# Optimization experiments

Hardware: AMD Instinct MI355X
Metric: run time of the kernel (lower is better)

The kernel has to match this reference:

```python
import jax, jax.numpy as jnp
import numpy as np

L, N, D, E, KD = 4, 40000, 128, 320000, 16
DECAY, N_ITER, EPS = 0.5, 3, 1e-5


def setup_inputs() -> dict:
    key = jax.random.key(0)
    ks = jax.random.split(key, 16)
    s = 0.05
    return {
        "x": jax.random.normal(ks[0], (L, N, D), jnp.float32),
        "edge_rows": jax.random.randint(ks[1], (E,), 0, N, jnp.int32),
        "edge_cols": jax.random.randint(ks[2], (E,), 0, N, jnp.int32),
        "edge_vals": jax.random.uniform(ks[3], (E,), jnp.float32) * 0.1,
        "sage_W": jax.random.normal(ks[4], (D, D), jnp.float32) * s,
        "sage_b": jnp.zeros((D,), jnp.float32),
        "sage_agg_W": jax.random.normal(ks[5], (D, D), jnp.float32) * s,
        "key_W": jax.random.normal(ks[6], (D, KD), jnp.float32) * s,
        "query_W": jax.random.normal(ks[7], (D, KD), jnp.float32) * s,
        "value_W": jax.random.normal(ks[8], (D, D), jnp.float32) * s,
        "attn_ln_g": jnp.ones((D,), jnp.float32),
        "attn_ln_b": jnp.zeros((D,), jnp.float32),
        "lin_W": jax.random.normal(ks[9], (D, D), jnp.float32) * s,
        "lin_b": jnp.zeros((D,), jnp.float32),
        "ln_g": jnp.ones((D,), jnp.float32),
        "ln_b": jnp.zeros((D,), jnp.float32),
    }


def _layernorm(x, g, b):
    mu = jnp.mean(x, axis=-1, keepdims=True)
    var = jnp.mean((x - mu) ** 2, axis=-1, keepdims=True)
    return (x - mu) * jax.lax.rsqrt(var + EPS) * g + b


def _spmm(rows, cols, vals, x2d):
    # sparse [N,N] @ dense [N,F]: out[r] = sum_e vals[e] * x2d[cols[e]] for rows[e]==r
    return jax.ops.segment_sum(vals[:, None] * x2d[cols], rows, num_segments=N)


def reference(x, edge_rows, edge_cols, edge_vals, sage_W, sage_b, sage_agg_W,
              key_W, query_W, value_W, attn_ln_g, attn_ln_b,
              lin_W, lin_b, ln_g, ln_b):
    # x: [L, N, D]
    x2d = jnp.transpose(x, (1, 0, 2)).reshape(N, L * D)  # [N, L*D]

    # ---- SAGEConv ----
    proj = x @ sage_W + sage_b
    agg = _spmm(edge_rows, edge_cols, edge_vals, x2d)
    agg = jnp.transpose(agg.reshape(N, L, D), (1, 0, 2)) @ sage_agg_W
    sage_out = jax.nn.silu(proj + agg)

    # ---- RetentiveAttention ----
    weights = jnp.mean((x @ key_W) * (x @ query_W), axis=-1, keepdims=True)
    x_acc = x
    cur = x2d
    for _ in range(1, N_ITER):
        cur = _spmm(edge_rows, edge_cols, edge_vals, cur * DECAY)
        xr = jnp.transpose(cur.reshape(N, L, D), (1, 0, 2))  # [L, N, D]
        weights = weights + jnp.mean((xr @ key_W) * (xr @ query_W), axis=-1, keepdims=True)
        x_acc = x_acc + xr
    attn_out = _layernorm((x_acc @ value_W) * weights, attn_ln_g, attn_ln_b)

    # ---- GPSConv fusion ----
    y = jax.nn.silu((sage_out + attn_out) @ lin_W + lin_b)
    return _layernorm(y, ln_g, ln_b)
```

## Files before the change

kernel.cpp:

```cpp
#include <hip/hip_runtime.h>
#include <math.h>

#define LL 4
#define NN 40000
#define DD 128
#define EE 320000
#define ROWS (LL*NN)
#define ND (NN*DD)
#define EPS_LN 1e-5f

typedef __attribute__((ext_vector_type(8))) short bf16x8;
typedef __attribute__((ext_vector_type(4))) short s16x4;
typedef __attribute__((ext_vector_type(4))) float f32x4;

#define OFF_CNT      0
#define OFF_ROWPTR   40000
#define OFF_ROWOFS   80004
#define OFF_CCOLS    120004
#define OFF_CVALS    440004
#define OFF_WBF      760004
#define OFF_A        829636
#define OFF_B        (OFF_A + ROWS*DD/2)

#define WB_W0  0
#define WB_W1  32768
#define WB_WV  65536
#define WB_WL  98304
#define WB_K   131072
#define WB_Q   135168
#define WB_LO_BIG 16384
#define WB_LO_KQ  2048
#define WB_LOGICAL 69632

__device__ __forceinline__ unsigned fu(float f) { union { float f; unsigned u; } v; v.f = f; return v.u; }
__device__ __forceinline__ float uf(unsigned u) { union { unsigned u; float f; } v; v.u = u; return v.f; }

__device__ __forceinline__ short f2bf(float f) {
    unsigned u = fu(f);
    unsigned r = u + 0x7fffu + ((u >> 16) & 1u);
    return (short)(r >> 16);
}
__device__ __forceinline__ float bf2f(short h) { return uf(((unsigned)(unsigned short)h) << 16); }
__device__ __forceinline__ void splitbf(float v, short& h, short& l) {
    h = f2bf(v);
    l = f2bf(v - bf2f(h));
}

__device__ __forceinline__ unsigned pack_hi(float a, float b) {
    return (fu(a) >> 16) | (fu(b) & 0xffff0000u);
}
__device__ __forceinline__ float resid(float a) {
    return a - uf(fu(a) & 0xffff0000u);
}

union FragU { bf16x8 v; unsigned u[4]; };

__global__ void k_hist(const int* __restrict__ rows, int* __restrict__ cnt) {
    int e = blockIdx.x * 256 + threadIdx.x;
    if (e < EE) atomicAdd(&cnt[rows[e]], 1);
}

__global__ __launch_bounds__(1024) void k_scan(const int* __restrict__ cnt,
                                               int* __restrict__ row_ptr,
                                               int* __restrict__ row_ofs) {
    __shared__ int wtot[16];
    __shared__ int s_carry;
    int tid = threadIdx.x;
    int lane = tid & 63, wid = tid >> 6;
    if (tid == 0) s_carry = 0;
    __syncthreads();
    for (int base = 0; base <= NN; base += 1024) {
        int i = base + tid;
        int v = (i < NN) ? cnt[i] : 0;
        int incl = v;
        #pragma unroll
        for (int off = 1; off < 64; off <<= 1) {
            int t = __shfl_up(incl, off);
            if (lane >= off) incl += t;
        }
        if (lane == 63) wtot[wid] = incl;
        __syncthreads();
        if (wid == 0) {
            int w = (lane < 16) ? wtot[lane] : 0;
            #pragma unroll
            for (int off = 1; off < 16; off <<= 1) {
                int t = __shfl_up(w, off);
                if (lane >= off) w += t;
            }
            if (lane < 16) wtot[lane] = w;
        }
        __syncthreads();
        int carry = s_carry;
        int wofs = (wid > 0) ? wtot[wid - 1] : 0;
        int excl = carry + wofs + incl - v;
        if (i <= NN) {
            row_ptr[i] = excl;
            if (i < NN) row_ofs[i] = excl;
        }
        __syncthreads();
        if (tid == 0) s_carry = carry + wtot[15];
        __syncthreads();
    }
}

__global__ void k_scatter(const int* __restrict__ rows, const int* __restrict__ cols,
                          const float* __restrict__ vals, int* __restrict__ row_ofs,
                          int* __restrict__ csr_cols, float* __restrict__ csr_vals) {
    int e = blockIdx.x * 256 + threadIdx.x;
    if (e < EE) {
        int r = rows[e];
        int p = atomicAdd(&row_ofs[r], 1);
        csr_cols[p] = cols[e];
        csr_vals[p] = vals[e];
    }
}

__global__ __launch_bounds__(128) void k_spmm_f32(const float* __restrict__ in,
                                                  const int* __restrict__ row_ptr,
                                                  const int* __restrict__ ccols,
                                                  const float* __restrict__ cvals,
                                                  short* __restrict__ out) {
    int r = blockIdx.x;
    int tid = threadIdx.x;
    int l = tid >> 5;
    int d4 = (tid & 31) * 4;
    const float* inl = in + (size_t)l * ND + d4;
    f32x4 acc = {0.f, 0.f, 0.f, 0.f};
    int e0 = row_ptr[r], e1 = row_ptr[r + 1];
    int e = e0;
    for (; e + 1 < e1; e += 2) {
        int c0 = ccols[e], c1 = ccols[e + 1];
        float v0 = cvals[e], v1 = cvals[e + 1];
        f32x4 x0 = *(const f32x4*)(inl + (size_t)c0 * DD);
        f32x4 x1 = *(const f32x4*)(inl + (size_t)c1 * DD);
        acc += v0 * x0;
        acc += v1 * x1;
    }
    if (e < e1) {
        int c = ccols[e];
        float v = cvals[e];
        acc += v * *(const f32x4*)(inl + (size_t)c * DD);
    }
    s16x4 o;
    o[0] = f2bf(acc[0]); o[1] = f2bf(acc[1]); o[2] = f2bf(acc[2]); o[3] = f2bf(acc[3]);
    *(s16x4*)(out + (size_t)l * ND + (size_t)r * DD + d4) = o;
}

__global__ __launch_bounds__(128) void k_spmm_bf16(const short* __restrict__ in,
                                                   const int* __restrict__ row_ptr,
                                                   const int* __restrict__ ccols,
                                                   const float* __restrict__ cvals,
                                                   short* __restrict__ out) {
    int r = blockIdx.x;
    int tid = threadIdx.x;
    int l = tid >> 5;
    int d4 = (tid & 31) * 4;
    const short* inl = in + (size_t)l * ND + d4;
    f32x4 acc = {0.f, 0.f, 0.f, 0.f};
    int e0 = row_ptr[r], e1 = row_ptr[r + 1];
    int e = e0;
    for (; e + 1 < e1; e += 2) {
        int c0 = ccols[e], c1 = ccols[e + 1];
        float v0 = cvals[e], v1 = cvals[e + 1];
        s16x4 x0 = *(const s16x4*)(inl + (size_t)c0 * DD);
        s16x4 x1 = *(const s16x4*)(inl + (size_t)c1 * DD);
        #pragma unroll
        for (int j = 0; j < 4; ++j) {
            acc[j] += v0 * bf2f(x0[j]);
            acc[j] += v1 * bf2f(x1[j]);
        }
    }
    if (e < e1) {
        int c = ccols[e];
        float v = cvals[e];
        s16x4 xv = *(const s16x4*)(inl + (size_t)c * DD);
        #pragma unroll
        for (int j = 0; j < 4; ++j) acc[j] += v * bf2f(xv[j]);
    }
    s16x4 o;
    o[0] = f2bf(acc[0]); o[1] = f2bf(acc[1]); o[2] = f2bf(acc[2]); o[3] = f2bf(acc[3]);
    *(s16x4*)(out + (size_t)l * ND + (size_t)r * DD + d4) = o;
}

__global__ void k_prep(const float* __restrict__ W0, const float* __restrict__ W1,
                       const float* __restrict__ Wv, const float* __restrict__ Wl,
                       const float* __restrict__ Kw, const float* __restrict__ Qw,
                       short* __restrict__ o) {
    int t = blockIdx.x * 256 + threadIdx.x;
    if (t >= WB_LOGICAL) return;
    float v;
    int hi_idx, lo_idx;
    if (t < 65536) {
        int m = t >> 14, idx = t & 16383;
        int nn = idx >> 7, kk = idx & 127;
        const float* M = (m == 0) ? W0 : (m == 1) ? W1 : (m == 2) ? Wv : Wl;
        v = M[kk * 128 + nn];
        hi_idx = m * 32768 + idx;
        lo_idx = hi_idx + WB_LO_BIG;
    } else {
        int t2 = t - 65536;
        int sel = t2 >> 11;
        int idx = t2 & 2047;
        int nn = idx >> 7, kk = idx & 127;
        const float* M = sel ? Qw : Kw;
        v = M[kk * 16 + nn];
        hi_idx = WB_K + sel * 4096 + idx;
        lo_idx = hi_idx + WB_LO_KQ;
    }
    short h, l;
    splitbf(v, h, l);
    o[hi_idx] = h;
    o[lo_idx] = l;
}

#define MFMA(a, b, c) __builtin_amdgcn_mfma_f32_16x16x32_bf16(a, b, c, 0, 0, 0)

__global__ __launch_bounds__(256) void k_dense(
    const float* __restrict__ x, const short* __restrict__ A, const short* __restrict__ B,
    const short* __restrict__ wbf,
    const float* __restrict__ sage_b, const float* __restrict__ attn_g,
    const float* __restrict__ attn_b, const float* __restrict__ lin_b,
    const float* __restrict__ ln_g, const float* __restrict__ ln_b,
    float* __restrict__ out)
{
    __shared__ float zs[4][16][132];
    const int tid = threadIdx.x;
    const int w = tid >> 6;
    const int lane = tid & 63;
    const int n = lane & 15;
    const int q = lane >> 4;
    const size_t rowA = (size_t)blockIdx.x * 64 + w * 16 + n;

    bf16x8 xh[4], ah[4], ch[4];
    f32x4 kx = {0,0,0,0}, qx = {0,0,0,0};
    f32x4 ka = {0,0,0,0}, qa = {0,0,0,0};
    f32x4 kb = {0,0,0,0}, qb = {0,0,0,0};

    {
        const float* xp = x + rowA * 128 + q * 8;
        const short* ap = A + rowA * 128 + q * 8;
        const short* bp = B + rowA * 128 + q * 8;
        const short* Kp = wbf + WB_K + n * 128 + q * 8;
        const short* Qp = wbf + WB_Q + n * 128 + q * 8;
        #pragma unroll
        for (int s = 0; s < 4; ++s) {
            f32x4 x0 = *(const f32x4*)(xp + s * 32);
            f32x4 x1 = *(const f32x4*)(xp + s * 32 + 4);
            bf16x8 av = *(const bf16x8*)(ap + s * 32);
            bf16x8 bv = *(const bf16x8*)(bp + s * 32);

            f32x4 c0, c1;
            #pragma unroll
            for (int j = 0; j < 4; ++j) {
                c0[j] = x0[j] + 0.5f * bf2f(av[j])     + 0.25f * bf2f(bv[j]);
                c1[j] = x1[j] + 0.5f * bf2f(av[j + 4]) + 0.25f * bf2f(bv[j + 4]);
            }

            FragU fxh, fxl, fch;
            #pragma unroll
            for (int i = 0; i < 2; ++i) {
                fxh.u[i]     = pack_hi(x0[2*i], x0[2*i+1]);
                fxh.u[i + 2] = pack_hi(x1[2*i], x1[2*i+1]);
                fxl.u[i]     = pack_hi(resid(x0[2*i]), resid(x0[2*i+1]));
                fxl.u[i + 2] = pack_hi(resid(x1[2*i]), resid(x1[2*i+1]));
                fch.u[i]     = pack_hi(c0[2*i], c0[2*i+1]);
                fch.u[i + 2] = pack_hi(c1[2*i], c1[2*i+1]);
            }
            xh[s] = fxh.v; ah[s] = av; ch[s] = fch.v;

            bf16x8 bkh = *(const bf16x8*)(Kp + s * 32);
            bf16x8 bkl = *(const bf16x8*)(Kp + WB_LO_KQ + s * 32);
            bf16x8 bqh = *(const bf16x8*)(Qp + s * 32);
            bf16x8 bql = *(const bf16x8*)(Qp + WB_LO_KQ + s * 32);
            kx = MFMA(fxh.v, bkh, kx); kx = MFMA(fxl.v, bkh, kx); kx = MFMA(fxh.v, bkl, kx);
            qx = MFMA(fxh.v, bqh, qx); qx = MFMA(fxl.v, bqh, qx); qx = MFMA(fxh.v, bql, qx);
            ka = MFMA(av, bkh, ka); qa = MFMA(av, bqh, qa);
            kb = MFMA(bv, bkh, kb); qb = MFMA(bv, bqh, qb);
        }
    }

    f32x4 wts;
    #pragma unroll
    for (int r = 0; r < 4; ++r) {
        float p = kx[r] * qx[r] + 0.25f * (ka[r] * qa[r]) + 0.0625f * (kb[r] * qb[r]);
        p += __shfl_xor(p, 1);
        p += __shfl_xor(p, 2);
        p += __shfl_xor(p, 4);
        p += __shfl_xor(p, 8);
        wts[r] = p * (1.f / 16.f);
    }

    f32x4 S[8];
    #pragma unroll
    for (int t = 0; t < 8; ++t) {
        float bv = sage_b[t * 16 + n];
        S[t] = (f32x4){bv, bv, bv, bv};
    }
    #pragma unroll
    for (int s = 0; s < 4; ++s) {
        #pragma unroll
        for (int t = 0; t < 8; ++t) {
            bf16x8 w0h = *(const bf16x8*)(wbf + WB_W0 + (t * 16 + n) * 128 + s * 32 + q * 8);
            S[t] = MFMA(xh[s], w0h, S[t]);
            bf16x8 w1h = *(const bf16x8*)(wbf + WB_W1 + (t * 16 + n) * 128 + s * 32 + q * 8);
            S[t] = MFMA(ah[s], w1h, S[t]);
        }
    }
    #pragma unroll
    for (int t = 0; t < 8; ++t)
        #pragma unroll
        for (int r = 0; r < 4; ++r) {
            float v = S[t][r];
            S[t][r] = v / (1.f + __expf(-v));
        }

    f32x4 V[8];
    #pragma unroll
    for (int t = 0; t < 8; ++t) V[t] = (f32x4){0.f, 0.f, 0.f, 0.f};
    #pragma unroll
    for (int s = 0; s < 4; ++s)
        #pragma unroll
        for (int t = 0; t < 8; ++t) {
            bf16x8 wvh = *(const bf16x8*)(wbf + WB_WV + (t * 16 + n) * 128 + s * 32 + q * 8);
            V[t] = MFMA(ch[s], wvh, V[t]);
        }
    f32x4 s1 = {0,0,0,0}, s2 = {0,0,0,0};
    #pragma unroll
    for (int t = 0; t < 8; ++t)
        #pragma unroll
        for (int r = 0; r < 4; ++r) {
            float v = V[t][r] * wts[r];
            V[t][r] = v;
            s1[r] += v; s2[r] += v * v;
        }
    #pragma unroll
    for (int r = 0; r < 4; ++r) {
        float a1 = s1[r], a2 = s2[r];
        a1 += __shfl_xor(a1, 1); a2 += __shfl_xor(a2, 1);
        a1 += __shfl_xor(a1, 2); a2 += __shfl_xor(a2, 2);
        a1 += __shfl_xor(a1, 4); a2 += __shfl_xor(a2, 4);
        a1 += __shfl_xor(a1, 8); a2 += __shfl_xor(a2, 8);
        s1[r] = a1; s2[r] = a2;
    }
    #pragma unroll
    for (int t = 0; t < 8; ++t) {
        float g = attn_g[t * 16 + n];
        float bb = attn_b[t * 16 + n];
        #pragma unroll
        for (int r = 0; r < 4; ++r) {
            float mu = s1[r] * (1.f / 128.f);
            float var = s2[r] * (1.f / 128.f) - mu * mu;
            float rs = rsqrtf(var + EPS_LN);
            zs[w][q * 4 + r][t * 16 + n] = S[t][r] + (V[t][r] - mu) * rs * g + bb;
        }
    }
    __syncthreads();

    bf16x8 zh[4];
    {
        const float* zrow = &zs[w][n][0];
        #pragma unroll
        for (int s = 0; s < 4; ++s) {
            f32x4 z0 = *(const f32x4*)(zrow + s * 32 + q * 8);
            f32x4 z1 = *(const f32x4*)(zrow + s * 32 + q * 8 + 4);
            FragU f;
            #pragma unroll
            for (int i = 0; i < 2; ++i) {
                f.u[i]     = pack_hi(z0[2*i], z0[2*i+1]);
                f.u[i + 2] = pack_hi(z1[2*i], z1[2*i+1]);
            }
            zh[s] = f.v;
        }
    }
    f32x4 F[8];
    #pragma unroll
    for (int t = 0; t < 8; ++t) {
        float bv = lin_b[t * 16 + n];
        F[t] = (f32x4){bv, bv, bv, bv};
    }
    #pragma unroll
    for (int s = 0; s < 4; ++s)
        #pragma unroll
        for (int t = 0; t < 8; ++t) {
            bf16x8 wlh = *(const bf16x8*)(wbf + WB_WL + (t * 16 + n) * 128 + s * 32 + q * 8);
            F[t] = MFMA(zh[s], wlh, F[t]);
        }
    f32x4 t1 = {0,0,0,0}, t2 = {0,0,0,0};
    #pragma unroll
    for (int t = 0; t < 8; ++t)
        #pragma unroll
        for (int r = 0; r < 4; ++r) {
            float v = F[t][r];
            v = v / (1.f + __expf(-v));
            F[t][r] = v;
            t1[r] += v; t2[r] += v * v;
        }
    #pragma unroll
    for (int r = 0; r < 4; ++r) {
        float a1 = t1[r], a2 = t2[r];
        a1 += __shfl_xor(a1, 1); a2 += __shfl_xor(a2, 1);
        a1 += __shfl_xor(a1, 2); a2 += __shfl_xor(a2, 2);
        a1 += __shfl_xor(a1, 4); a2 += __shfl_xor(a2, 4);
        a1 += __shfl_xor(a1, 8); a2 += __shfl_xor(a2, 8);
        t1[r] = a1; t2[r] = a2;
    }
    #pragma unroll
    for (int t = 0; t < 8; ++t) {
        float g = ln_g[t * 16 + n];
        float bb = ln_b[t * 16 + n];
        #pragma unroll
        for (int r = 0; r < 4; ++r) {
            float mu = t1[r] * (1.f / 128.f);
            float var = t2[r] * (1.f / 128.f) - mu * mu;
            float rs = rsqrtf(var + EPS_LN);
            size_t row = (size_t)blockIdx.x * 64 + w * 16 + q * 4 + r;
            out[row * 128 + t * 16 + n] = (F[t][r] - mu) * rs * g + bb;
        }
    }
}

extern "C" void kernel_launch(void* const* d_in, const int* in_sizes, int n_in,
                              void* d_out, int out_size, void* d_ws, size_t ws_size,
                              hipStream_t stream) {
    const float* x       = (const float*)d_in[0];
    const int*   erows   = (const int*)d_in[1];
    const int*   ecols   = (const int*)d_in[2];
    const float* evals   = (const float*)d_in[3];
    const float* sage_W  = (const float*)d_in[4];
    const float* sage_b  = (const float*)d_in[5];
    const float* sage_aW = (const float*)d_in[6];
    const float* key_W   = (const float*)d_in[7];
    const float* query_W = (const float*)d_in[8];
    const float* value_W = (const float*)d_in[9];
    const float* attn_g  = (const float*)d_in[10];
    const float* attn_b  = (const float*)d_in[11];
    const float* lin_W   = (const float*)d_in[12];
    const float* lin_b   = (const float*)d_in[13];
    const float* ln_g    = (const float*)d_in[14];
    const float* ln_b    = (const float*)d_in[15];
    float* out = (float*)d_out;

    int*   wsi = (int*)d_ws;
    float* wsf = (float*)d_ws;
    int*   cnt      = wsi + OFF_CNT;
    int*   row_ptr  = wsi + OFF_ROWPTR;
    int*   row_ofs  = wsi + OFF_ROWOFS;
    int*   csr_cols = wsi + OFF_CCOLS;
    float* csr_vals = wsf + OFF_CVALS;
    short* wbf      = (short*)(wsf + OFF_WBF);
    short* Abf      = (short*)(wsf + OFF_A);
    short* Bbf      = (short*)(wsf + OFF_B);

    hipMemsetAsync(cnt, 0, NN * sizeof(int), stream);
    k_hist<<<(EE + 255) / 256, 256, 0, stream>>>(erows, cnt);
    k_prep<<<(WB_LOGICAL + 255) / 256, 256, 0, stream>>>(sage_W, sage_aW, value_W, lin_W,
                                                         key_W, query_W, wbf);
    k_scan<<<1, 1024, 0, stream>>>(cnt, row_ptr, row_ofs);
    k_scatter<<<(EE + 255) / 256, 256, 0, stream>>>(erows, ecols, evals, row_ofs, csr_cols, csr_vals);

    k_spmm_f32<<<NN, 128, 0, stream>>>(x, row_ptr, csr_cols, csr_vals, Abf);
    k_spmm_bf16<<<NN, 128, 0, stream>>>(Abf, row_ptr, csr_cols, csr_vals, Bbf);

    k_dense<<<ROWS / 64, 256, 0, stream>>>(x, Abf, Bbf, wbf, sage_b, attn_g, attn_b,
                                           lin_b, ln_g, ln_b, out);
}
```

Before: 602.2 us.

## Cast x to bf16 for SpMM, parallelize scan, unroll gathers, bf16 swizzled LDS

Replaces the single-block serial prefix scan with a three-kernel multi-block scan. Adds a pre-cast of x to bf16 so the first SpMM gathers half the bytes, and unrolls the SpMM edge loop by 8/4 to get more gathers in flight. In the dense kernel, the fp32 LDS staging buffer with a __syncthreads becomes a per-wave bf16 XOR-swizzled buffer with no block barrier. It adds an extra cast pass over x, and the first SpMM input now loses precision to bf16.

```diff
diff --git a/kernel.cpp b/kernel.cpp
--- a/kernel.cpp
+++ b/kernel.cpp
@@ -21,6 +21,7 @@
 #define OFF_WBF      760004
 #define OFF_A        829636
 #define OFF_B        (OFF_A + ROWS*DD/2)
+#define OFF_XBF      (OFF_B + ROWS*DD/2)
 
 #define WB_W0  0
 #define WB_W1  32768
@@ -60,47 +61,60 @@
     if (e < EE) atomicAdd(&cnt[rows[e]], 1);
 }
 
-__global__ __launch_bounds__(1024) void k_scan(const int* __restrict__ cnt,
-                                               int* __restrict__ row_ptr,
-                                               int* __restrict__ row_ofs) {
+__global__ __launch_bounds__(1024) void k_scan1(const int* __restrict__ cnt,
+                                                int* __restrict__ row_ptr,
+                                                int* __restrict__ bsum) {
     __shared__ int wtot[16];
-    __shared__ int s_carry;
-    int tid = threadIdx.x;
-    int lane = tid & 63, wid = tid >> 6;
-    if (tid == 0) s_carry = 0;
+    int tid = threadIdx.x, lane = tid & 63, wid = tid >> 6;
+    int i = blockIdx.x * 1024 + tid;
+    int v = (i < NN) ? cnt[i] : 0;
+    int incl = v;
+    #pragma unroll
+    for (int off = 1; off < 64; off <<= 1) {
+        int t = __shfl_up(incl, off);
+        if (lane >= off) incl += t;
+    }
+    if (lane == 63) wtot[wid] = incl;
     __syncthreads();
-    for (int base = 0; base <= NN; base += 1024) {
-        int i = base + tid;
-        int v = (i < NN) ? cnt[i] : 0;
-        int incl = v;
-        #pragma unroll
-        for (int off = 1; off < 64; off <<= 1) {
-            int t = __shfl_up(incl, off);
-            if (lane >= off) incl += t;
-        }
-        if (lane == 63) wtot[wid] = incl;
-        __syncthreads();
-        if (wid == 0) {
-            int w = (lane < 16) ? wtot[lane] : 0;
-            #pragma unroll
-            for (int off = 1; off < 16; off <<= 1) {
-                int t = __shfl_up(w, off);
-                if (lane >= off) w += t;
-            }
-            if (lane < 16) wtot[lane] = w;
-        }
-        __syncthreads();
-        int carry = s_carry;
-        int wofs = (wid > 0) ? wtot[wid - 1] : 0;
-        int excl = carry + wofs + incl - v;
-        if (i <= NN) {
-            row_ptr[i] = excl;
-            if (i < NN) row_ofs[i] = excl;
-        }
-        __syncthreads();
-        if (tid == 0) s_carry = carry + wtot[15];
-        __syncthreads();
-    }
+    if (wid == 0) {
+        int wv = (lane < 16) ? wtot[lane] : 0;
+        #pragma unroll
+        for (int off = 1; off < 16; off <<= 1) {
+            int t = __shfl_up(wv, off);
+            if (lane >= off) wv += t;
+        }
+        if (lane < 16) wtot[lane] = wv;
+    }
+    __syncthreads();
+    int excl = ((wid > 0) ? wtot[wid - 1] : 0) + incl - v;
+    if (i < NN) row_ptr[i] = excl;
+    if (tid == 0) bsum[blockIdx.x] = wtot[15];
+}
+
+__global__ void k_scan2(const int* __restrict__ bsum, int* __restrict__ bofs) {
+    int lane = threadIdx.x;
+    int v = (lane < 40) ? bsum[lane] : 0;
+    int incl = v;
+    #pragma unroll
+    for (int off = 1; off < 64; off <<= 1) {
+        int t = __shfl_up(incl, off);
+        if (lane >= off) incl += t;
+    }
+    if (lane < 40) bofs[lane] = incl - v;
+    if (lane == 39) bofs[40] = incl;
+}
+
+__global__ __launch_bounds__(1024) void k_scan3(const int* __restrict__ bofs,
+                                                int* __restrict__ row_ptr,
+                                                int* __restrict__ row_ofs) {
+    int i = blockIdx.x * 1024 + threadIdx.x;
+    int add = bofs[blockIdx.x];
+    if (i < NN) {
+        int v = row_ptr[i] + add;
+        row_ptr[i] = v;
+        row_ofs[i] = v;
+    }
+    if (i == NN) row_ptr[NN] = bofs[40];
 }
 
 __global__ void k_scatter(const int* __restrict__ rows, const int* __restrict__ cols,
@@ -115,42 +129,21 @@
     }
 }
 
-__global__ __launch_bounds__(128) void k_spmm_f32(const float* __restrict__ in,
-                                                  const int* __restrict__ row_ptr,
-                                                  const int* __restrict__ ccols,
-                                                  const float* __restrict__ cvals,
-                                                  short* __restrict__ out) {
-    int r = blockIdx.x;
-    int tid = threadIdx.x;
-    int l = tid >> 5;
-    int d4 = (tid & 31) * 4;
-    const float* inl = in + (size_t)l * ND + d4;
-    f32x4 acc = {0.f, 0.f, 0.f, 0.f};
-    int e0 = row_ptr[r], e1 = row_ptr[r + 1];
-    int e = e0;
-    for (; e + 1 < e1; e += 2) {
-        int c0 = ccols[e], c1 = ccols[e + 1];
-        float v0 = cvals[e], v1 = cvals[e + 1];
-        f32x4 x0 = *(const f32x4*)(inl + (size_t)c0 * DD);
-        f32x4 x1 = *(const f32x4*)(inl + (size_t)c1 * DD);
-        acc += v0 * x0;
-        acc += v1 * x1;
-    }
-    if (e < e1) {
-        int c = ccols[e];
-        float v = cvals[e];
-        acc += v * *(const f32x4*)(inl + (size_t)c * DD);
-    }
-    s16x4 o;
-    o[0] = f2bf(acc[0]); o[1] = f2bf(acc[1]); o[2] = f2bf(acc[2]); o[3] = f2bf(acc[3]);
-    *(s16x4*)(out + (size_t)l * ND + (size_t)r * DD + d4) = o;
-}
-
-__global__ __launch_bounds__(128) void k_spmm_bf16(const short* __restrict__ in,
-                                                   const int* __restrict__ row_ptr,
-                                                   const int* __restrict__ ccols,
-                                                   const float* __restrict__ cvals,
-                                                   short* __restrict__ out) {
+__global__ __launch_bounds__(256) void k_xcast(const float* __restrict__ x, short* __restrict__ o) {
+    size_t i = ((size_t)blockIdx.x * 256 + threadIdx.x) * 8;
+    f32x4 a = *(const f32x4*)(x + i);
+    f32x4 b = *(const f32x4*)(x + i + 4);
+    bf16x8 r;
+    #pragma unroll
+    for (int j = 0; j < 4; ++j) { r[j] = f2bf(a[j]); r[j + 4] = f2bf(b[j]); }
+    *(bf16x8*)(o + i) = r;
+}
+
+__global__ __launch_bounds__(128) void k_spmm(const short* __restrict__ in,
+                                              const int* __restrict__ row_ptr,
+                                              const int* __restrict__ ccols,
+                                              const float* __restrict__ cvals,
+                                              short* __restrict__ out) {
     int r = blockIdx.x;
     int tid = threadIdx.x;
     int l = tid >> 5;
@@ -159,23 +152,46 @@
     f32x4 acc = {0.f, 0.f, 0.f, 0.f};
     int e0 = row_ptr[r], e1 = row_ptr[r + 1];
     int e = e0;
-    for (; e + 1 < e1; e += 2) {
+    for (; e + 8 <= e1; e += 8) {
+        float v[8]; s16x4 xv[8];
+        #pragma unroll
+        for (int j = 0; j < 8; ++j) {
+            int c = ccols[e + j];
+            v[j] = cvals[e + j];
+            xv[j] = *(const s16x4*)(inl + (size_t)c * DD);
+        }
+        #pragma unroll
+        for (int j = 0; j < 8; ++j)
+            #pragma unroll
+            for (int k = 0; k < 4; ++k) acc[k] += v[j] * bf2f(xv[j][k]);
+    }
+    for (; e + 4 <= e1; e += 4) {
+        float v[4]; s16x4 xv[4];
+        #pragma unroll
+        for (int j = 0; j < 4; ++j) {
+            int c = ccols[e + j];
+            v[j] = cvals[e + j];
+            xv[j] = *(const s16x4*)(inl + (size_t)c * DD);
+        }
+        #pragma unroll
+        for (int j = 0; j < 4; ++j)
+            #pragma unroll
+            for (int k = 0; k < 4; ++k) acc[k] += v[j] * bf2f(xv[j][k]);
+    }
+    for (; e + 2 <= e1; e += 2) {
         int c0 = ccols[e], c1 = ccols[e + 1];
         float v0 = cvals[e], v1 = cvals[e + 1];
         s16x4 x0 = *(const s16x4*)(inl + (size_t)c0 * DD);
         s16x4 x1 = *(const s16x4*)(inl + (size_t)c1 * DD);
         #pragma unroll
-        for (int j = 0; j < 4; ++j) {
-            acc[j] += v0 * bf2f(x0[j]);
-            acc[j] += v1 * bf2f(x1[j]);
-        }
+        for (int k = 0; k < 4; ++k) { acc[k] += v0 * bf2f(x0[k]); acc[k] += v1 * bf2f(x1[k]); }
     }
     if (e < e1) {
         int c = ccols[e];
         float v = cvals[e];
         s16x4 xv = *(const s16x4*)(inl + (size_t)c * DD);
         #pragma unroll
-        for (int j = 0; j < 4; ++j) acc[j] += v * bf2f(xv[j]);
+        for (int k = 0; k < 4; ++k) acc[k] += v * bf2f(xv[k]);
     }
     s16x4 o;
     o[0] = f2bf(acc[0]); o[1] = f2bf(acc[1]); o[2] = f2bf(acc[2]); o[3] = f2bf(acc[3]);
@@ -223,13 +239,14 @@
     const float* __restrict__ ln_g, const float* __restrict__ ln_b,
     float* __restrict__ out)
 {
-    __shared__ float zs[4][16][132];
+    __shared__ short zs[4][16 * 128];
     const int tid = threadIdx.x;
     const int w = tid >> 6;
     const int lane = tid & 63;
     const int n = lane & 15;
     const int q = lane >> 4;
     const size_t rowA = (size_t)blockIdx.x * 64 + w * 16 + n;
+    char* zb = (char*)&zs[0][0] + w * 4096;
 
     bf16x8 xh[4], ah[4], ch[4];
     f32x4 kx = {0,0,0,0}, qx = {0,0,0,0};
@@ -351,26 +368,18 @@
             float mu = s1[r] * (1.f / 128.f);
             float var = s2[r] * (1.f / 128.f) - mu * mu;
             float rs = rsqrtf(var + EPS_LN);
-            zs[w][q * 4 + r][t * 16 + n] = S[t][r] + (V[t][r] - mu) * rs * g + bb;
-        }
-    }
-    __syncthreads();
+            float zval = S[t][r] + (V[t][r] - mu) * rs * g + bb;
+            int row = q * 4 + r;
+            int byte = (row * 256 + (t * 16 + n) * 2) ^ ((row & 7) << 4);
+            *(short*)(zb + byte) = f2bf(zval);
+        }
+    }
 
     bf16x8 zh[4];
-    {
-        const float* zrow = &zs[w][n][0];
-        #pragma unroll
-        for (int s = 0; s < 4; ++s) {
-            f32x4 z0 = *(const f32x4*)(zrow + s * 32 + q * 8);
-            f32x4 z1 = *(const f32x4*)(zrow + s * 32 + q * 8 + 4);
-            FragU f;
-            #pragma unroll
-            for (int i = 0; i < 2; ++i) {
-                f.u[i]     = pack_hi(z0[2*i], z0[2*i+1]);
-                f.u[i + 2] = pack_hi(z1[2*i], z1[2*i+1]);
-            }
-            zh[s] = f.v;
-        }
+    #pragma unroll
+    for (int s = 0; s < 4; ++s) {
+        int byte = (n * 256 + s * 64 + q * 16) ^ ((n & 7) << 4);
+        zh[s] = *(const bf16x8*)(zb + byte);
     }
     f32x4 F[8];
     #pragma unroll
@@ -450,16 +459,22 @@
     short* wbf      = (short*)(wsf + OFF_WBF);
     short* Abf      = (short*)(wsf + OFF_A);
     short* Bbf      = (short*)(wsf + OFF_B);
+    short* Xbf      = (short*)(wsf + OFF_XBF);
+    int*   bsum     = (int*)(wsf + OFF_A);
+    int*   bofs     = bsum + 64;
 
     hipMemsetAsync(cnt, 0, NN * sizeof(int), stream);
     k_hist<<<(EE + 255) / 256, 256, 0, stream>>>(erows, cnt);
     k_prep<<<(WB_LOGICAL + 255) / 256, 256, 0, stream>>>(sage_W, sage_aW, value_W, lin_W,
                                                          key_W, query_W, wbf);
-    k_scan<<<1, 1024, 0, stream>>>(cnt, row_ptr, row_ofs);
+    k_xcast<<<ROWS * DD / (256 * 8), 256, 0, stream>>>(x, Xbf);
+    k_scan1<<<40, 1024, 0, stream>>>(cnt, row_ptr, bsum);
+    k_scan2<<<1, 64, 0, stream>>>(bsum, bofs);
+    k_scan3<<<40, 1024, 0, stream>>>(bofs, row_ptr, row_ofs);
     k_scatter<<<(EE + 255) / 256, 256, 0, stream>>>(erows, ecols, evals, row_ofs, csr_cols, csr_vals);
 
-    k_spmm_f32<<<NN, 128, 0, stream>>>(x, row_ptr, csr_cols, csr_vals, Abf);
-    k_spmm_bf16<<<NN, 128, 0, stream>>>(Abf, row_ptr, csr_cols, csr_vals, Bbf);
+    k_spmm<<<NN, 128, 0, stream>>>(Xbf, row_ptr, csr_cols, csr_vals, Abf);
+    k_spmm<<<NN, 128, 0, stream>>>(Abf, row_ptr, csr_cols, csr_vals, Bbf);
 
     k_dense<<<ROWS / 64, 256, 0, stream>>>(x, Abf, Bbf, wbf, sage_b, attn_g, attn_b,
                                            lin_b, ln_g, ln_b, out);
```

Measured after the change: 565.4 us. -6.1%, faster.
